# Performance work log

Measured on AMD Instinct MI355X. Metric: run time of the kernel, lower is better.

## Reference

```python
import jax, jax.numpy as jnp
import numpy as np

N = 262144
H = 128
NB = 3  # alpha, xp, yp branches


def _lin_init(key, out_d, in_d, shape):
    bound = 1.0 / np.sqrt(in_d)
    return jax.random.uniform(key, shape, jnp.float32, -bound, bound)


def setup_inputs() -> dict:
    key = jax.random.key(0)
    ks = jax.random.split(key, 9)
    t = jax.random.normal(ks[0], (N,), jnp.float32)
    W1 = _lin_init(ks[1], H, 1, (NB, H, 1))
    b1 = _lin_init(ks[2], H, 1, (NB, H))
    W2 = _lin_init(ks[3], H, H, (NB, H, H))
    b2 = _lin_init(ks[4], H, H, (NB, H))
    W3 = _lin_init(ks[5], H, H, (NB, H, H))
    b3 = _lin_init(ks[6], H, H, (NB, H))
    W4 = _lin_init(ks[7], 1, H, (NB, 1, H))
    b4 = _lin_init(ks[8], 1, H, (NB, 1))
    return {"t": t, "W1": W1, "b1": b1, "W2": W2, "b2": b2,
            "W3": W3, "b3": b3, "W4": W4, "b4": b4}


def _mlp(t, w1, c1, w2, c2, w3, c3, w4, c4):
    # t: [N]; one branch: 1 -> H -> H -> H -> 1 with relu on hidden layers
    h = jax.nn.relu(t[:, None] * w1[:, 0][None, :] + c1)  # [N, H]
    h = jax.nn.relu(h @ w2.T + c2)                        # [N, H]
    h = jax.nn.relu(h @ w3.T + c3)                        # [N, H]
    return (h @ w4.T + c4)[:, 0]                          # [N]


def _post(v, dt, neg):
    # dt is d(v)/dt per element (= the torch double-backward result)
    s = -1.0 if neg else 1.0
    dsign = s * jnp.sign(v - v[0]) * dt
    d0 = jnp.where(dsign[1] >= 0, jnp.abs(dt[0:1]), -jnp.abs(dt[0:1]))
    dsign = jnp.concatenate([d0, dsign[1:]])
    vv = s * jnp.abs(v - v[0])
    return vv, dsign


def reference(t, W1, b1, W2, b2, W3, b3, W4, b4):
    ones = jnp.ones_like(t)

    def branch(w1, c1, w2, c2, w3, c3, w4, c4):
        # value and analytic d/dt via forward-mode JVP (tangent of t is 1)
        return jax.jvp(lambda tt: _mlp(tt, w1, c1, w2, c2, w3, c3, w4, c4),
                       (t,), (ones,))

    vals, dts = jax.vmap(branch)(W1, b1, W2, b2, W3, b3, W4, b4)  # [3, N] each
    alpha, da = _post(vals[0], dts[0], False)
    xp, dx = _post(vals[1], dts[1], True)
    yp, dy = _post(vals[2], dts[2], False)
    return (alpha, xp, yp, da, dx, dy)
```

## Files before the change

### kernel.cpp

```cpp
#include <hip/hip_runtime.h>
#include <math.h>

#define N_ELEM 262144
#define HDIM 128
#define M_TILE 64
#define DEADBAND 2e-5f
#define GAPBAND 4e-5f
#define REFNOISE 1e-6
#define THR_FRAC 0.0198f
#define EPS_1 2e-6f
#define EPS_A 1e-5f
#define CMAX 9.0e-3f
#define CAP 16384

typedef __attribute__((ext_vector_type(8))) short bf16x8;
typedef __attribute__((ext_vector_type(4))) short bf16x4;
typedef __attribute__((ext_vector_type(4))) float f32x4;
typedef __attribute__((ext_vector_type(16))) float f32x16;
typedef __attribute__((ext_vector_type(4))) unsigned u32x4;
typedef __attribute__((ext_vector_type(2))) unsigned u32x2;

static __device__ __forceinline__ unsigned short f2bf(float x) {
    unsigned u = __float_as_uint(x);
    unsigned r = u + 0x7FFF + ((u >> 16) & 1);
    return (unsigned short)(r >> 16);
}
static __device__ __forceinline__ float bf2f(unsigned short h) {
    return __uint_as_float(((unsigned)h) << 16);
}

static __device__ __forceinline__ unsigned cvtpk_bf16(float lo, float hi) {
    unsigned r;
    asm("v_cvt_pk_bf16_f32 %0, %1, %2" : "=v"(r) : "v"(lo), "v"(hi));
    return r;
}
static __device__ __forceinline__ void psplit2(float x0, float x1,
        unsigned& w0, unsigned& w1) {
    w0 = cvtpk_bf16(x0, x1);
    float h0a = __uint_as_float(w0 << 16);
    float h0b = __uint_as_float(w0 & 0xFFFF0000u);
    w1 = cvtpk_bf16(x0 - h0a, x1 - h0b);
}
static __device__ __forceinline__ unsigned packbf(float lo, float hi) {
    return (unsigned)f2bf(lo) | ((unsigned)f2bf(hi) << 16);
}


__global__ void k_prep(const float* __restrict__ W2, const float* __restrict__ W3,
                       unsigned short* __restrict__ Wb0, unsigned short* __restrict__ Wb1,
                       unsigned short* __restrict__ Wb2) {
    int g = blockIdx.x * 256 + threadIdx.x;
    const float* src = (g >= 49152) ? W3 : W2;
    int r = (g >= 49152) ? g - 49152 : g;
    float w = src[r];
    unsigned short h0 = f2bf(w);
    float r1 = w - bf2f(h0);
    unsigned short h1 = f2bf(r1);
    Wb0[g] = h0; Wb1[g] = h1; Wb2[g] = f2bf(r1 - bf2f(h1));
}

__global__ __launch_bounds__(256, 3) void k_mlp(
    const float* __restrict__ t,  const float* __restrict__ W1,
    const float* __restrict__ b1, const float* __restrict__ b2,
    const float* __restrict__ b3, const float* __restrict__ W4,
    const float* __restrict__ b4,
    const unsigned short* __restrict__ Wb0, const unsigned short* __restrict__ Wb1,
    const unsigned short* __restrict__ Wb2,
    float* __restrict__ vf, float* __restrict__ out,
    unsigned* __restrict__ cnt, unsigned* __restrict__ list)
{
    __shared__ __align__(16) unsigned short Bv0[64 * 128];
    __shared__ __align__(16) unsigned short Bv1[64 * 128];
    __shared__ __align__(16) unsigned short Bt0[64 * 128];
    __shared__ unsigned char flg[64];

    const int tid  = threadIdx.x;
    const int wave = tid >> 6;
    const int lane = tid & 63;
    const int l31  = lane & 31;
    const int half = lane >> 5;
    const int b    = blockIdx.y;
    const int e0   = blockIdx.x * M_TILE;

    if (tid < 64) flg[tid] = 0;
    __syncthreads();

    {
        const int m  = tid >> 2;
        const int kb = (tid & 3) * 32;
        const int sw = (m & 7) << 3;
        const int mb = m << 7;
        float tval = t[e0 + m];
        const float* W1p = W1 + b * 128 + kb;
        const float* b1p = b1 + b * 128 + kb;
        unsigned char f = 0;
        #pragma unroll
        for (int kh = 0; kh < 4; ++kh) {
            f32x4 wA = *(const f32x4*)(W1p + kh * 8);
            f32x4 wB = *(const f32x4*)(W1p + kh * 8 + 4);
            f32x4 cA = *(const f32x4*)(b1p + kh * 8);
            f32x4 cB = *(const f32x4*)(b1p + kh * 8 + 4);
            float hv[8], ht[8];
            #pragma unroll
            for (int kk = 0; kk < 8; ++kk) {
                float w1 = (kk < 4) ? wA[kk] : wB[kk - 4];
                float bb = (kk < 4) ? cA[kk] : cB[kk - 4];
                float pre = fmaf(tval, w1, bb);
                if (fabsf(pre) < EPS_1) f = 1;
                hv[kk] = pre > 0.f ? pre : 0.f;
                ht[kk] = pre > 0.f ? w1 : 0.f;
            }
            u32x4 rv0, rv1, rt0;
            #pragma unroll
            for (int p = 0; p < 4; ++p) {
                unsigned s0, s1;
                psplit2(hv[2 * p], hv[2 * p + 1], s0, s1);
                rv0[p] = s0; rv1[p] = s1;
                rt0[p] = packbf(ht[2 * p], ht[2 * p + 1]);
            }
            const int idx = mb + ((kb + kh * 8) ^ sw);
            *(u32x4*)&Bv0[idx] = rv0;
            *(u32x4*)&Bv1[idx] = rv1;
            *(u32x4*)&Bt0[idx] = rt0;
        }
        if (f) flg[m] = 1;
    }
    __syncthreads();

    const int swz = (l31 & 7) << 3;
    #pragma unroll 1
    for (int lay = 0; lay < 2; ++lay) {
        const float* bias = (lay ? b3 : b2) + b * 128;

        const int wrow = (wave << 5) + l31;
        const int woff = ((lay * 3 + b) << 14) + (wrow << 7) + (half << 3);
        const unsigned short* pW0 = Wb0 + woff;
        const unsigned short* pW1 = Wb1 + woff;
        const unsigned short* pW2 = Wb2 + woff;

        f32x4 bias4[4];
        #pragma unroll
        for (int g = 0; g < 4; ++g)
            bias4[g] = *(const f32x4*)(bias + (wave << 5) + (g << 3) + (half << 2));

        f32x16 accv[2], acct[2];
        #pragma unroll
        for (int mm = 0; mm < 2; ++mm) {
            #pragma unroll
            for (int r = 0; r < 16; ++r) { accv[mm][r] = 0.f; acct[mm][r] = 0.f; }
        }

        #pragma unroll
        for (int ks = 0; ks < 8; ++ks) {
            bf16x8 w0 = *(const bf16x8*)(pW0 + (ks << 4));
            bf16x8 w1 = *(const bf16x8*)(pW1 + (ks << 4));
            bf16x8 w2 = *(const bf16x8*)(pW2 + (ks << 4));
            const int cx = ((ks << 4) + (half << 3)) ^ swz;
            #pragma unroll
            for (int mm = 0; mm < 2; ++mm) {
                const int idx = (mm << 12) + (l31 << 7) + cx;
                bf16x8 a0 = *(const bf16x8*)&Bv0[idx];
                bf16x8 a1 = *(const bf16x8*)&Bv1[idx];
                bf16x8 c0 = *(const bf16x8*)&Bt0[idx];
                accv[mm] = __builtin_amdgcn_mfma_f32_32x32x16_bf16(w2, a0, accv[mm], 0, 0, 0);
                accv[mm] = __builtin_amdgcn_mfma_f32_32x32x16_bf16(w1, a1, accv[mm], 0, 0, 0);
                accv[mm] = __builtin_amdgcn_mfma_f32_32x32x16_bf16(w1, a0, accv[mm], 0, 0, 0);
                accv[mm] = __builtin_amdgcn_mfma_f32_32x32x16_bf16(w0, a1, accv[mm], 0, 0, 0);
                accv[mm] = __builtin_amdgcn_mfma_f32_32x32x16_bf16(w0, a0, accv[mm], 0, 0, 0);
                acct[mm] = __builtin_amdgcn_mfma_f32_32x32x16_bf16(w1, c0, acct[mm], 0, 0, 0);
                acct[mm] = __builtin_amdgcn_mfma_f32_32x32x16_bf16(w0, c0, acct[mm], 0, 0, 0);
            }
        }
        __syncthreads();

        #pragma unroll
        for (int mm = 0; mm < 2; ++mm) {
            const int mb = (mm << 12) + (l31 << 7);
            const int m  = (mm << 5) + l31;
            #pragma unroll
            for (int g = 0; g < 4; ++g) {
                const int jc = (wave << 5) + (g << 3) + (half << 2);
                float hv[4], ht[4];
                #pragma unroll
                for (int r = 0; r < 4; ++r) {
                    float pre = accv[mm][g * 4 + r] + bias4[g][r];
                    float tp  = acct[mm][g * 4 + r];
                    if (fabsf(pre) < EPS_A) flg[m] = 1;
                    hv[r] = pre > 0.f ? pre : 0.f;
                    ht[r] = pre > 0.f ? tp : 0.f;
                }
                u32x2 p0, p1, q0;
                unsigned s0, s1;
                psplit2(hv[0], hv[1], s0, s1);
                p0[0] = s0; p1[0] = s1;
                psplit2(hv[2], hv[3], s0, s1);
                p0[1] = s0; p1[1] = s1;
                q0[0] = packbf(ht[0], ht[1]);
                q0[1] = packbf(ht[2], ht[3]);
                const int widx = mb + (jc ^ swz);
                *(u32x2*)&Bv0[widx] = p0;
                *(u32x2*)&Bv1[widx] = p1;
                *(u32x2*)&Bt0[widx] = q0;
            }
        }
        __syncthreads();
    }

    {
        const int m  = tid >> 2;
        const int tp = tid & 3;
        const int jb = tp * 32;
        const int sw = (m & 7) << 3;
        const int mb = m << 7;
        const float* W4p = W4 + b * 128 + jb;
        float pv = 0.f, pt = 0.f;
        #pragma unroll
        for (int c = 0; c < 4; ++c) {
            const int idx = mb + ((jb + c * 8) ^ sw);
            bf16x8 q0 = *(bf16x8*)&Bv0[idx];
            bf16x8 q1 = *(bf16x8*)&Bv1[idx];
            bf16x8 s0 = *(bf16x8*)&Bt0[idx];
            f32x4 wA = *(const f32x4*)(W4p + c * 8);
            f32x4 wB = *(const f32x4*)(W4p + c * 8 + 4);
            #pragma unroll
            for (int l = 0; l < 8; ++l) {
                float hv = bf2f((unsigned short)q0[l]) + bf2f((unsigned short)q1[l]);
                float ht = bf2f((unsigned short)s0[l]);
                float w = (l < 4) ? wA[l] : wB[l - 4];
                pv = fmaf(hv, w, pv);
                pt = fmaf(ht, w, pt);
            }
        }
        pv += __shfl_xor(pv, 1); pv += __shfl_xor(pv, 2);
        pt += __shfl_xor(pt, 1); pt += __shfl_xor(pt, 2);
        if (tp == 0) {
            vf[b * N_ELEM + e0 + m] = pv + b4[b];
            out[3 * N_ELEM + b * N_ELEM + e0 + m] = pt;
        }
    }

    if (tid < 64 && flg[tid]) {
        unsigned idx = atomicAdd(cnt, 1u);
        if (idx < CAP) list[idx] = (unsigned)(b * N_ELEM + e0 + tid);
    }
}


__global__ void k_exact01(
    const float* __restrict__ t,  const float* __restrict__ W1,
    const float* __restrict__ b1, const float* __restrict__ W2,
    const float* __restrict__ b2, const float* __restrict__ W3,
    const float* __restrict__ b3, const float* __restrict__ W4,
    const float* __restrict__ b4, double* __restrict__ sc)
{
    __shared__ double h[128], h2[128], red[128];
    int j = threadIdx.x;
    for (int b = 0; b < 3; ++b)
        for (int e = 0; e < 2; ++e) {
            double tv = (double)t[e];
            double pre = fma(tv, (double)W1[b * 128 + j], (double)b1[b * 128 + j]);
            h[j] = pre > 0.0 ? pre : 0.0;
            __syncthreads();
            {
                const float* W = W2 + b * 16384 + j * 128;
                double acc = (double)b2[b * 128 + j];
                for (int k0 = 0; k0 < 128; k0 += 4) {
                    f32x4 wq = *(const f32x4*)(W + k0);
                    #pragma unroll
                    for (int kk = 0; kk < 4; ++kk)
                        acc = fma(h[k0 + kk], (double)wq[kk], acc);
                }
                h2[j] = acc > 0.0 ? acc : 0.0;
            }
            __syncthreads();
            {
                const float* W = W3 + b * 16384 + j * 128;
                double acc = (double)b3[b * 128 + j];
                for (int k0 = 0; k0 < 128; k0 += 4) {
                    f32x4 wq = *(const f32x4*)(W + k0);
                    #pragma unroll
                    for (int kk = 0; kk < 4; ++kk)
                        acc = fma(h2[k0 + kk], (double)wq[kk], acc);
                }
                h[j] = acc > 0.0 ? acc : 0.0;
            }
            __syncthreads();
            red[j] = h[j] * (double)W4[b * 128 + j];
            __syncthreads();
            for (int s = 64; s > 0; s >>= 1) {
                if (j < s) red[j] += red[j + s];
                __syncthreads();
            }
            if (j == 0) sc[b * 4 + e] = red[0] + (double)b4[b];
            __syncthreads();
        }
}

__global__ void k_gmax_flag(const float* __restrict__ vf,
                            const float* __restrict__ out,
                            const double* __restrict__ sc,
                            unsigned* __restrict__ gm,
                            unsigned* __restrict__ cnt,
                            unsigned* __restrict__ list) {
    __shared__ unsigned red[4];
    int g = blockIdx.x * 256 + threadIdx.x;
    int b = g / N_ELEM;
    float v0 = (float)sc[b * 4];
    float gap = fabsf(vf[g] - v0);
    float dt  = fabsf(out[3 * N_ELEM + g]);
    if (gap < GAPBAND) {
        unsigned idx = atomicAdd(cnt, 1u);
        if (idx < CAP) list[idx] = (unsigned)g;
    }
    unsigned v = __float_as_uint(fmaxf(gap, dt));
    #pragma unroll
    for (int s = 1; s < 64; s <<= 1) {
        unsigned o = (unsigned)__shfl_xor((int)v, s);
        v = v > o ? v : o;
    }
    int wave = threadIdx.x >> 6;
    if ((threadIdx.x & 63) == 0) red[wave] = v;
    __syncthreads();
    if (threadIdx.x == 0) {
        unsigned m = red[0];
        #pragma unroll
        for (int w = 1; w < 4; ++w) m = m > red[w] ? m : red[w];
        atomicMax(gm, m);
    }
}

__global__ __launch_bounds__(128) void k_fix(
    const float* __restrict__ t,  const float* __restrict__ W1,
    const float* __restrict__ b1, const float* __restrict__ W2,
    const float* __restrict__ b2, const float* __restrict__ W3,
    const float* __restrict__ b3, const float* __restrict__ W4,
    const float* __restrict__ b4,
    const unsigned* __restrict__ cnt, const unsigned* __restrict__ list,
    float* __restrict__ out, float* __restrict__ vf,
    double* __restrict__ vex, float* __restrict__ fixdt)
{
    __shared__ double hT[128], hA[128], hB[128];
    __shared__ float  tT[128], tA[128], tB[128];
    __shared__ double nhT[128], nhA[128], nhB[128];
    __shared__ float  ntT[128], ntA[128], ntB[128];
    unsigned c = *cnt; if (c > CAP) c = CAP;
    unsigned n = blockIdx.x;
    if (n >= c) return;
    unsigned g = list[n];
    int b = g / N_ELEM;
    int i = g - b * N_ELEM;
    int j = threadIdx.x;

    double tv = (double)t[i];
    float  w1 = W1[b * 128 + j];
    double pre = fma(tv, (double)w1, (double)b1[b * 128 + j]);
    bool amb = fabs(pre) < (double)EPS_1;
    bool mT = pre > 0.0;
    bool mA = amb ? false : mT;
    bool mB = amb ? true  : mT;
    hT[j] = mT ? pre : 0.0;  tT[j] = mT ? w1 : 0.f;
    hA[j] = mA ? pre : 0.0;  tA[j] = mA ? w1 : 0.f;
    hB[j] = mB ? pre : 0.0;  tB[j] = mB ? w1 : 0.f;
    __syncthreads();

    #pragma unroll 1
    for (int layer = 0; layer < 2; ++layer) {
        const float* W = (layer ? W3 : W2) + b * 16384 + j * 128;
        double bb = (double)((layer ? b3 : b2)[b * 128 + j]);
        double pT = bb, pA = bb, pB = bb;
        float  zT = 0.f, zA = 0.f, zB = 0.f;
        for (int k0 = 0; k0 < 128; k0 += 4) {
            f32x4 wq = *(const f32x4*)(W + k0);
            #pragma unroll
            for (int kk = 0; kk < 4; ++kk) {
                int k = k0 + kk;
                float wf = wq[kk];
                double wd = (double)wf;
                pT = fma(hT[k], wd, pT); zT = fmaf(tT[k], wf, zT);
                pA = fma(hA[k], wd, pA); zA = fmaf(tA[k], wf, zA);
                pB = fma(hB[k], wd, pB); zB = fmaf(tB[k], wf, zB);
            }
        }
        bool mTl  = pT > 0.0;
        bool ambl = (fabs(pA) < (double)EPS_A) || (fabs(pB) < (double)EPS_A);
        bool mAl  = ambl ? false : (pA > 0.0);
        bool mBl  = ambl ? true  : (pB > 0.0);
        nhT[j] = mTl ? pT : 0.0;  ntT[j] = mTl ? zT : 0.f;
        nhA[j] = mAl ? pA : 0.0;  ntA[j] = mAl ? zA : 0.f;
        nhB[j] = mBl ? pB : 0.0;  ntB[j] = mBl ? zB : 0.f;
        __syncthreads();
        hT[j] = nhT[j]; tT[j] = ntT[j];
        hA[j] = nhA[j]; tA[j] = ntA[j];
        hB[j] = nhB[j]; tB[j] = ntB[j];
        __syncthreads();
    }

    if (j == 0) {
        double vT = 0.0; float dT = 0.f, dA = 0.f, dB = 0.f;
        for (int k0 = 0; k0 < 128; k0 += 4) {
            f32x4 wq = *(const f32x4*)(W4 + b * 128 + k0);
            #pragma unroll
            for (int kk = 0; kk < 4; ++kk) {
                int k = k0 + kk;
                float w4 = wq[kk];
                vT = fma(hT[k], (double)w4, vT);
                dT = fmaf(tT[k], w4, dT);
                dA = fmaf(tA[k], w4, dA);
                dB = fmaf(tB[k], w4, dB);
            }
        }
        vT += (double)b4[b];
        float delta = dB - dA;
        float dtfix = (fabsf(delta) < CMAX) ? 0.5f * (dA + dB) : dT;
        out[3 * N_ELEM + g] = dtfix;
        fixdt[n] = dtfix;
        vex[n]   = vT;
        vf[g]    = (float)vT;
    }
}

__global__ void k_scal(const float* __restrict__ out, double* __restrict__ sc) {
    int b = threadIdx.x;
    if (b < 3) {
        sc[b * 4 + 2] = (double)out[3 * N_ELEM + b * N_ELEM];
        sc[b * 4 + 3] = (double)out[3 * N_ELEM + b * N_ELEM + 1];
    }
}

__global__ void k_post(const float* __restrict__ vf,
                       float* __restrict__ out,
                       const double* __restrict__ sc,
                       const unsigned* __restrict__ gm) {
    int g = blockIdx.x * 256 + threadIdx.x;
    int b = g / N_ELEM;
    int i = g - b * N_ELEM;
    float s = (b == 1) ? -1.f : 1.f;
    float thr = THR_FRAC * __uint_as_float(*gm);

    float v0 = (float)sc[b * 4];
    float v  = vf[b * N_ELEM + i];
    float dt = out[3 * N_ELEM + b * N_ELEM + i];

    float d   = v - v0;
    float gap = fabsf(d);
    float ds;
    if (i == 0) {
        double v1  = sc[b * 4 + 1];
        double dt0 = sc[b * 4 + 2];
        double dt1 = sc[b * 4 + 3];
        double d1  = v1 - sc[b * 4];
        double sg1 = (d1 > 0.0) ? 1.0 : ((d1 < 0.0) ? -1.0 : 0.0);
        double ds1 = (double)s * sg1 * dt1;
        ds = (float)((ds1 >= 0.0) ? fabs(dt0) : -fabs(dt0));
        if (fabs(dt0) < (double)thr) ds = 0.f;
        gap = 0.f;
    } else {
        float sgn = (d > 0.f) ? 1.f : ((d < 0.f) ? -1.f : 0.f);
        ds = s * sgn * dt;
        if (gap < DEADBAND && fabsf(dt) < thr) ds = 0.f;
    }
    out[b * N_ELEM + i]              = s * gap;
    out[3 * N_ELEM + b * N_ELEM + i] = ds;
}

__global__ void k_fix2(const unsigned* __restrict__ cnt,
                       const unsigned* __restrict__ list,
                       const double* __restrict__ vex,
                       const float* __restrict__ fixdt,
                       const double* __restrict__ sc,
                       const unsigned* __restrict__ gm,
                       float* __restrict__ out) {
    unsigned c = *cnt; if (c > CAP) c = CAP;
    unsigned n = blockIdx.x * 64 + threadIdx.x;
    if (n >= c) return;
    unsigned g = list[n];
    int b = g / N_ELEM;
    int i = g - b * N_ELEM;
    if (i == 0) return;
    double s = (b == 1) ? -1.0 : 1.0;
    double gapd = vex[n] - sc[b * 4];
    float  dt   = fixdt[n];
    float  thr  = THR_FRAC * __uint_as_float(*gm);
    double sgn = (gapd > 0.0) ? 1.0 : ((gapd < 0.0) ? -1.0 : 0.0);
    float ds = (float)(s * sgn) * dt;
    if (fabs(gapd) < REFNOISE && fabsf(dt) < thr) ds = 0.f;
    out[b * N_ELEM + i]              = (float)(s * fabs(gapd));
    out[3 * N_ELEM + b * N_ELEM + i] = ds;
}

extern "C" void kernel_launch(void* const* d_in, const int* in_sizes, int n_in,
                              void* d_out, int out_size, void* d_ws, size_t ws_size,
                              hipStream_t stream) {
    const float* t  = (const float*)d_in[0];
    const float* W1 = (const float*)d_in[1];
    const float* b1 = (const float*)d_in[2];
    const float* W2 = (const float*)d_in[3];
    const float* b2 = (const float*)d_in[4];
    const float* W3 = (const float*)d_in[5];
    const float* b3 = (const float*)d_in[6];
    const float* W4 = (const float*)d_in[7];
    const float* b4 = (const float*)d_in[8];
    float* out = (float*)d_out;
    char* ws   = (char*)d_ws;
    unsigned short* Wb0 = (unsigned short*)ws;
    unsigned short* Wb1 = (unsigned short*)(ws + 196608);
    float*    vf    = (float*)(ws + 393216);
    double*   sc    = (double*)(ws + 3538944);
    unsigned* gm    = (unsigned*)(ws + 3539040);
    unsigned* cnt   = (unsigned*)(ws + 3539044);
    unsigned* list  = (unsigned*)(ws + 3539048);
    double*   vex   = (double*)(ws + 3604592);
    float*    fixdt = (float*)(ws + 3735664);
    unsigned short* Wb2 = (unsigned short*)(ws + 3801200);

    hipMemsetAsync(gm, 0, 8, stream);
    k_prep<<<384, 256, 0, stream>>>(W2, W3, Wb0, Wb1, Wb2);
    k_mlp<<<dim3(N_ELEM / M_TILE, 3), 256, 0, stream>>>(t, W1, b1, b2, b3, W4, b4,
                                                        Wb0, Wb1, Wb2, vf, out, cnt, list);
    k_exact01<<<1, 128, 0, stream>>>(t, W1, b1, W2, b2, W3, b3, W4, b4, sc);
    k_gmax_flag<<<(3 * N_ELEM) / 256, 256, 0, stream>>>(vf, out, sc, gm, cnt, list);
    k_fix<<<CAP, 128, 0, stream>>>(t, W1, b1, W2, b2, W3, b3, W4, b4,
                                   cnt, list, out, vf, vex, fixdt);
    k_scal<<<1, 64, 0, stream>>>(out, sc);
    k_post<<<(3 * N_ELEM) / 256, 256, 0, stream>>>(vf, out, sc, gm);
    k_fix2<<<CAP / 64, 64, 0, stream>>>(cnt, list, vex, fixdt, sc, gm, out);
}
```

Measured before the change: 1.070 ms.

## Fuse final linear layer into layer-3 MFMA epilogue, skip LDS writeback

The second hidden layer is unrolled out of the loop, and its epilogue applies bias and ReLU and then takes the dot product with W4 directly in registers. Partial sums are reduced across the two half-waves with a shuffle and across the four waves through a small shared buffer. This removes the bf16 split and pack of layer-3 activations, their LDS store, a sync, and the separate reload pass for the output layer, and it keeps layer-3 activations in fp32 rather than split bf16. The cost is extra shared arrays, one more sync, and different summation order and precision.

```diff
diff --git a/kernel.cpp b/kernel.cpp
--- a/kernel.cpp
+++ b/kernel.cpp
@@ -72,6 +72,8 @@
     __shared__ __align__(16) unsigned short Bv0[64 * 128];
     __shared__ __align__(16) unsigned short Bv1[64 * 128];
     __shared__ __align__(16) unsigned short Bt0[64 * 128];
+    __shared__ float redv[4][2][32];
+    __shared__ float redt[4][2][32];
     __shared__ unsigned char flg[64];
 
     const int tid  = threadIdx.x;
@@ -127,16 +129,15 @@
     }
     __syncthreads();
 
-    const int swz = (l31 & 7) << 3;
-    #pragma unroll 1
-    for (int lay = 0; lay < 2; ++lay) {
-        const float* bias = (lay ? b3 : b2) + b * 128;
-
-        const int wrow = (wave << 5) + l31;
-        const int woff = ((lay * 3 + b) << 14) + (wrow << 7) + (half << 3);
+    const int swz  = (l31 & 7) << 3;
+    const int wrow = (wave << 5) + l31;
+
+    {
+        const int woff = (b << 14) + (wrow << 7) + (half << 3);
         const unsigned short* pW0 = Wb0 + woff;
         const unsigned short* pW1 = Wb1 + woff;
         const unsigned short* pW2 = Wb2 + woff;
+        const float* bias = b2 + b * 128;
 
         f32x4 bias4[4];
         #pragma unroll
@@ -207,35 +208,92 @@
     }
 
     {
-        const int m  = tid >> 2;
-        const int tp = tid & 3;
-        const int jb = tp * 32;
-        const int sw = (m & 7) << 3;
-        const int mb = m << 7;
-        const float* W4p = W4 + b * 128 + jb;
-        float pv = 0.f, pt = 0.f;
-        #pragma unroll
-        for (int c = 0; c < 4; ++c) {
-            const int idx = mb + ((jb + c * 8) ^ sw);
-            bf16x8 q0 = *(bf16x8*)&Bv0[idx];
-            bf16x8 q1 = *(bf16x8*)&Bv1[idx];
-            bf16x8 s0 = *(bf16x8*)&Bt0[idx];
-            f32x4 wA = *(const f32x4*)(W4p + c * 8);
-            f32x4 wB = *(const f32x4*)(W4p + c * 8 + 4);
-            #pragma unroll
-            for (int l = 0; l < 8; ++l) {
-                float hv = bf2f((unsigned short)q0[l]) + bf2f((unsigned short)q1[l]);
-                float ht = bf2f((unsigned short)s0[l]);
-                float w = (l < 4) ? wA[l] : wB[l - 4];
-                pv = fmaf(hv, w, pv);
-                pt = fmaf(ht, w, pt);
-            }
-        }
-        pv += __shfl_xor(pv, 1); pv += __shfl_xor(pv, 2);
-        pt += __shfl_xor(pt, 1); pt += __shfl_xor(pt, 2);
-        if (tp == 0) {
-            vf[b * N_ELEM + e0 + m] = pv + b4[b];
-            out[3 * N_ELEM + b * N_ELEM + e0 + m] = pt;
+        const int woff = ((3 + b) << 14) + (wrow << 7) + (half << 3);
+        const unsigned short* pW0 = Wb0 + woff;
+        const unsigned short* pW1 = Wb1 + woff;
+        const unsigned short* pW2 = Wb2 + woff;
+        const float* bias = b3 + b * 128;
+        const float* W4b  = W4 + b * 128;
+
+        f32x4 bias4[4], w4q[4];
+        #pragma unroll
+        for (int g = 0; g < 4; ++g) {
+            const int jr = (wave << 5) + (g << 3) + (half << 2);
+            bias4[g] = *(const f32x4*)(bias + jr);
+            w4q[g]   = *(const f32x4*)(W4b + jr);
+        }
+
+        f32x16 accv[2], acct[2];
+        #pragma unroll
+        for (int mm = 0; mm < 2; ++mm) {
+            #pragma unroll
+            for (int r = 0; r < 16; ++r) { accv[mm][r] = 0.f; acct[mm][r] = 0.f; }
+        }
+
+        #pragma unroll
+        for (int ks = 0; ks < 8; ++ks) {
+            bf16x8 w0 = *(const bf16x8*)(pW0 + (ks << 4));
+            bf16x8 w1 = *(const bf16x8*)(pW1 + (ks << 4));
+            bf16x8 w2 = *(const bf16x8*)(pW2 + (ks << 4));
+            const int cx = ((ks << 4) + (half << 3)) ^ swz;
+            #pragma unroll
+            for (int mm = 0; mm < 2; ++mm) {
+                const int idx = (mm << 12) + (l31 << 7) + cx;
+                bf16x8 a0 = *(const bf16x8*)&Bv0[idx];
+                bf16x8 a1 = *(const bf16x8*)&Bv1[idx];
+                bf16x8 c0 = *(const bf16x8*)&Bt0[idx];
+                accv[mm] = __builtin_amdgcn_mfma_f32_32x32x16_bf16(w2, a0, accv[mm], 0, 0, 0);
+                accv[mm] = __builtin_amdgcn_mfma_f32_32x32x16_bf16(w1, a1, accv[mm], 0, 0, 0);
+                accv[mm] = __builtin_amdgcn_mfma_f32_32x32x16_bf16(w1, a0, accv[mm], 0, 0, 0);
+                accv[mm] = __builtin_amdgcn_mfma_f32_32x32x16_bf16(w0, a1, accv[mm], 0, 0, 0);
+                accv[mm] = __builtin_amdgcn_mfma_f32_32x32x16_bf16(w0, a0, accv[mm], 0, 0, 0);
+                acct[mm] = __builtin_amdgcn_mfma_f32_32x32x16_bf16(w1, c0, acct[mm], 0, 0, 0);
+                acct[mm] = __builtin_amdgcn_mfma_f32_32x32x16_bf16(w0, c0, acct[mm], 0, 0, 0);
+            }
+        }
+
+        float pvv0 = 0.f, pvv1 = 0.f, ptt0 = 0.f, ptt1 = 0.f;
+        #pragma unroll
+        for (int g = 0; g < 4; ++g) {
+            #pragma unroll
+            for (int r = 0; r < 4; ++r) {
+                float w4 = w4q[g][r];
+                {
+                    float pre = accv[0][g * 4 + r] + bias4[g][r];
+                    float tp  = acct[0][g * 4 + r];
+                    if (fabsf(pre) < EPS_A) flg[l31] = 1;
+                    float hv = pre > 0.f ? pre : 0.f;
+                    float ht = pre > 0.f ? tp : 0.f;
+                    pvv0 = fmaf(hv, w4, pvv0);
+                    ptt0 = fmaf(ht, w4, ptt0);
+                }
+                {
+                    float pre = accv[1][g * 4 + r] + bias4[g][r];
+                    float tp  = acct[1][g * 4 + r];
+                    if (fabsf(pre) < EPS_A) flg[32 + l31] = 1;
+                    float hv = pre > 0.f ? pre : 0.f;
+                    float ht = pre > 0.f ? tp : 0.f;
+                    pvv1 = fmaf(hv, w4, pvv1);
+                    ptt1 = fmaf(ht, w4, ptt1);
+                }
+            }
+        }
+        pvv0 += __shfl_xor(pvv0, 32); pvv1 += __shfl_xor(pvv1, 32);
+        ptt0 += __shfl_xor(ptt0, 32); ptt1 += __shfl_xor(ptt1, 32);
+        if (half == 0) {
+            redv[wave][0][l31] = pvv0; redv[wave][1][l31] = pvv1;
+            redt[wave][0][l31] = ptt0; redt[wave][1][l31] = ptt1;
+        }
+        __syncthreads();
+
+        if (tid < 64) {
+            const int mm = tid >> 5, c = tid & 31;
+            float pv = (redv[0][mm][c] + redv[1][mm][c])
+                     + (redv[2][mm][c] + redv[3][mm][c]);
+            float pt = (redt[0][mm][c] + redt[1][mm][c])
+                     + (redt[2][mm][c] + redt[3][mm][c]);
+            vf[b * N_ELEM + e0 + tid] = pv + b4[b];
+            out[3 * N_ELEM + b * N_ELEM + e0 + tid] = pt;
         }
     }
 
```

Result: faster. 1.034 ms (-3.3%).
